# Kernel tuning notes

Hardware: AMD Instinct MI355X
Metric: run time of the kernel (lower is better)

The kernel has to match this reference:

```python
import jax, jax.numpy as jnp
import numpy as np

N = 100000      # nodes
E = 1600000     # edges
D = 64          # embedding_dim
NB = 5000       # boundary nodes
BLOCK = (8, 8, 8)
NBLK = BLOCK[0] * BLOCK[1] * BLOCK[2]  # 512 supernodes


def _segment_softmax(logits, seg, num):
    # jraph.segment_softmax: stable per-segment softmax
    m = jax.ops.segment_max(logits, seg, num_segments=num)
    e = jnp.exp(logits - m[seg])
    s = jax.ops.segment_sum(e, seg, num_segments=num)
    return e / s[seg]


def _gat(x, s, r, W, A, num):
    h = x @ W                       # [n, D]
    hs, hr = h[s], h[r]             # [E, D] gathers
    score = jax.nn.leaky_relu(jnp.concatenate([hs, hr], axis=-1) @ A)  # [E, 1]
    coeff = _segment_softmax(score, r, num)
    return jax.ops.segment_sum(hs * coeff, r, num_segments=num)        # [num, D]


def _graphnorm(x, gamma, beta, eps=1e-5):
    mean = jnp.mean(x, axis=0, keepdims=True)
    var = jnp.var(x, axis=0, keepdims=True)
    return gamma * (x - mean) / jnp.sqrt(var + eps) + beta


def setup_inputs() -> dict:
    key = jax.random.key(0)
    ks = jax.random.split(key, 16)

    def lecun(k, shape):
        return jax.random.normal(k, shape, jnp.float32) / jnp.sqrt(shape[0])

    return {
        "nodes": jax.random.normal(ks[0], (N, 7), jnp.float32),
        "senders": jax.random.randint(ks[1], (E,), 0, N, jnp.int32),
        "receivers": jax.random.randint(ks[2], (E,), 0, N, jnp.int32),
        "boundary_nodes": jax.random.randint(ks[3], (NB,), 0, N, jnp.int32),
        "disp_mean": jnp.zeros((3,), jnp.float32),
        "disp_std": jnp.ones((3,), jnp.float32),
        "embed_W": lecun(ks[4], (7, D)),
        "embed_b": jnp.zeros((D,), jnp.float32),
        "W1": lecun(ks[5], (D, D)),
        "A1": lecun(ks[6], (2 * D, 1)),
        "gamma1": jnp.ones((D,), jnp.float32),
        "beta1": jnp.zeros((D,), jnp.float32),
        "W2": lecun(ks[7], (D, D)),
        "A2": lecun(ks[8], (2 * D, 1)),
        "gamma2": jnp.ones((D,), jnp.float32),
        "beta2": jnp.zeros((D,), jnp.float32),
        "W3": lecun(ks[9], (D, D)),
        "A3": lecun(ks[10], (2 * D, 1)),
        "dec_W": lecun(ks[11], (D, 1)),
        "dec_b": jnp.zeros((1,), jnp.float32),
    }


def reference(nodes, senders, receivers, boundary_nodes, disp_mean, disp_std,
              embed_W, embed_b, W1, A1, gamma1, beta1, W2, A2, gamma2, beta2,
              W3, A3, dec_W, dec_b):
    coords = nodes[:, 0:3]
    # --- embedder: normalize boundary displacements, linear embed ---
    pos, disp, flag = nodes[:, 0:3], nodes[:, 3:6], nodes[:, 6:]
    b_disp = (disp[boundary_nodes] - disp_mean) / disp_std
    disp_n = disp.at[boundary_nodes].set(b_disp)
    x = jnp.concatenate([pos, disp_n, flag], axis=1) @ embed_W + embed_b  # [N, D]
    # --- GAT 1 + GraphNorm + silu + residual ---
    res1 = x
    x = _gat(x, senders, receivers, W1, A1, N)
    x = _graphnorm(x, gamma1, beta1)
    x = jax.nn.silu(x) + res1
    # --- BlockCoursening pooling ---
    dims = jnp.array(BLOCK)
    mn = jnp.min(coords, axis=0)
    mx = jnp.max(coords, axis=0)
    cell = (mx - mn) / dims
    gi = jnp.clip(jnp.floor((coords - mn) / cell).astype(jnp.int32), 0, dims - 1)
    bid = gi[:, 0] * (BLOCK[1] * BLOCK[2]) + gi[:, 1] * BLOCK[2] + gi[:, 2]  # [N]
    cnodes = jax.ops.segment_sum(x, bid, num_segments=NBLK)
    sizes = jax.ops.segment_sum(jnp.ones((N, 1), jnp.float32), bid, num_segments=NBLK)
    cnodes = cnodes / jnp.sqrt(sizes + 1e-10)
    bs, br = bid[senders], bid[receivers]
    # sorted-key dedup edge-weight mask (computed in source; unused by downstream GAT)
    keys = bs * NBLK + br
    idx = jnp.arange(E)
    sk, perm = jax.lax.sort_key_val(keys, idx)
    prev = jnp.concatenate([jnp.array([-1], sk.dtype), sk[:-1]])
    uniq = jnp.zeros((E,), bool).at[perm].set(sk != prev)
    edge_w = (uniq & (bs != br)).astype(jnp.float32)[:, None]  # noqa: F841 (dead in source too)
    # --- GAT 2 on coarsened graph + GraphNorm + silu + residual ---
    x2 = cnodes
    res2 = x2
    x2 = _gat(x2, bs, br, W2, A2, NBLK)
    x2 = _graphnorm(x2, gamma2, beta2)
    x2 = jax.nn.silu(x2) + res2
    # --- GAT 3 + residual ---
    res3 = x2
    x2 = _gat(x2, bs, br, W3, A3, NBLK)
    x2 = x2 + res3
    # --- decoder: sum-pool all nodes (single graph) -> linear -> scalar ---
    agg = jnp.sum(x2, axis=0, keepdims=True)  # segment_sum with one segment
    e = (agg @ dec_W + dec_b).squeeze()
    return e
```

## Files before the change

kernel.cpp:

```cpp
#include <hip/hip_runtime.h>
#include <hip/hip_bf16.h>

#define NN 100000
#define NE 1600000
#define NBN 5000
#define NCOARSE 512
#define NSB 391
#define NREP 8
#define NREP2 32

__device__ __forceinline__ unsigned f2ord(float f) {
    unsigned u = __float_as_uint(f);
    return (u & 0x80000000u) ? ~u : (u | 0x80000000u);
}
__device__ __forceinline__ float ord2f(unsigned u) {
    u = (u & 0x80000000u) ? (u & 0x7FFFFFFFu) : ~u;
    return __uint_as_float(u);
}
__device__ __forceinline__ float lrelu(float x) { return x > 0.f ? x : 0.01f * x; }

__global__ __launch_bounds__(256) void k_scatter(const int* __restrict__ bn, unsigned char* __restrict__ isb) {
    int i = blockIdx.x * 256 + threadIdx.x;
    if (i < NBN) isb[bn[i]] = 1;
}

__global__ __launch_bounds__(256) void k_embed(const float* __restrict__ nodes, const unsigned char* __restrict__ isb,
                                               const float* __restrict__ dmean, const float* __restrict__ dstd,
                                               const float* __restrict__ eW, const float* __restrict__ eb,
                                               float* __restrict__ x) {
    __shared__ float sW[448];
    __shared__ float sb[64];
    __shared__ float sm[3], sd[3];
    int t = threadIdx.x;
    for (int i = t; i < 448; i += 256) sW[i] = eW[i];
    if (t < 64) sb[t] = eb[t];
    if (t < 3) { sm[t] = dmean[t]; sd[t] = dstd[t]; }
    __syncthreads();
    int lane = t & 63, wv = t >> 6;
    int w = blockIdx.x * 4 + wv, nw = gridDim.x * 4;
    for (int n = w; n < NN; n += nw) {
        float row[7];
#pragma unroll
        for (int k = 0; k < 7; k++) row[k] = nodes[n * 7 + k];
        if (isb[n]) {
#pragma unroll
            for (int k = 0; k < 3; k++) row[3 + k] = (row[3 + k] - sm[k]) / sd[k];
        }
        float acc = sb[lane];
#pragma unroll
        for (int k = 0; k < 7; k++) acc += row[k] * sW[k * 64 + lane];
        x[n * 64 + lane] = acc;
    }
}

__global__ __launch_bounds__(256) void k_minmax(const float* __restrict__ nodes, unsigned* __restrict__ mn_ord,
                                                unsigned* __restrict__ mx_ord) {
    int tid = blockIdx.x * 256 + threadIdx.x;
    int stride = gridDim.x * 256;
    float mn[3] = {INFINITY, INFINITY, INFINITY};
    float mx[3] = {-INFINITY, -INFINITY, -INFINITY};
    for (int n = tid; n < NN; n += stride) {
#pragma unroll
        for (int k = 0; k < 3; k++) {
            float c = nodes[n * 7 + k];
            mn[k] = fminf(mn[k], c);
            mx[k] = fmaxf(mx[k], c);
        }
    }
#pragma unroll
    for (int off = 32; off; off >>= 1) {
#pragma unroll
        for (int k = 0; k < 3; k++) {
            mn[k] = fminf(mn[k], __shfl_down(mn[k], off));
            mx[k] = fmaxf(mx[k], __shfl_down(mx[k], off));
        }
    }
    if ((threadIdx.x & 63) == 0) {
#pragma unroll
        for (int k = 0; k < 3; k++) {
            atomicMin(&mn_ord[k], f2ord(mn[k]));
            atomicMax(&mx_ord[k], f2ord(mx[k]));
        }
    }
}

__global__ __launch_bounds__(256) void k_bid(const float* __restrict__ nodes, const unsigned* __restrict__ mn_ord,
                                             const unsigned* __restrict__ mx_ord, int* __restrict__ bid) {
    int n = blockIdx.x * 256 + threadIdx.x;
    if (n >= NN) return;
    int g[3];
#pragma unroll
    for (int k = 0; k < 3; k++) {
        float mn = ord2f(mn_ord[k]), mx = ord2f(mx_ord[k]);
        float cell = (mx - mn) / 8.0f;
        int gi = (int)floorf((nodes[n * 7 + k] - mn) / cell);
        gi = gi < 0 ? 0 : (gi > 7 ? 7 : gi);
        g[k] = gi;
    }
    bid[n] = g[0] * 64 + g[1] * 8 + g[2];
}

__global__ __launch_bounds__(256) void k_mm(const float* __restrict__ x, const float* __restrict__ W,
                                            const float* __restrict__ A, float* __restrict__ h,
                                            float* __restrict__ as_, float* __restrict__ ar_, int nrow) {
    __shared__ float sW[4096];
    __shared__ float sA[128];
    int t = threadIdx.x;
    for (int i = t; i < 4096; i += 256) sW[i] = W[i];
    if (t < 128) sA[t] = A[t];
    __syncthreads();
    int lane = t & 63, wv = t >> 6;
    int w = blockIdx.x * 4 + wv, nw = gridDim.x * 4;
    for (int n = w; n < nrow; n += nw) {
        const float* xr = x + (size_t)n * 64;
        float acc = 0.f;
#pragma unroll
        for (int k = 0; k < 64; k++) acc += xr[k] * sW[k * 64 + lane];
        h[(size_t)n * 64 + lane] = acc;
        float va = acc * sA[lane], vr = acc * sA[64 + lane];
#pragma unroll
        for (int off = 32; off; off >>= 1) {
            va += __shfl_down(va, off);
            vr += __shfl_down(vr, off);
        }
        if (lane == 0) { as_[n] = va; ar_[n] = vr; }
    }
}

__global__ __launch_bounds__(256) void k_deg(const int* __restrict__ re, unsigned* __restrict__ deg) {
    int e = blockIdx.x * 256 + threadIdx.x;
    if (e < NE) atomicAdd(&deg[re[e]], 1u);
}

__global__ __launch_bounds__(256) void k_scan1(const unsigned* __restrict__ deg, unsigned* __restrict__ rowptr,
                                               unsigned* __restrict__ partial) {
    __shared__ unsigned s[256];
    int t = threadIdx.x, i = blockIdx.x * 256 + t;
    unsigned v = (i < NN) ? deg[i] : 0u;
    s[t] = v;
    __syncthreads();
    for (int off = 1; off < 256; off <<= 1) {
        unsigned u = (t >= off) ? s[t - off] : 0u;
        __syncthreads();
        s[t] += u;
        __syncthreads();
    }
    if (i < NN) rowptr[i] = s[t] - v;
    if (t == 255) partial[blockIdx.x] = s[255];
}

__global__ __launch_bounds__(512) void k_scan2(unsigned* __restrict__ partial) {
    __shared__ unsigned s[512];
    int t = threadIdx.x;
    unsigned v = (t < NSB) ? partial[t] : 0u;
    s[t] = v;
    __syncthreads();
    for (int off = 1; off < 512; off <<= 1) {
        unsigned u = (t >= off) ? s[t - off] : 0u;
        __syncthreads();
        s[t] += u;
        __syncthreads();
    }
    if (t < NSB) partial[t] = s[t] - v;
}

__global__ __launch_bounds__(256) void k_scan3(unsigned* __restrict__ rowptr, const unsigned* __restrict__ partial,
                                               unsigned* __restrict__ cursor) {
    int t = threadIdx.x, i = blockIdx.x * 256 + t;
    if (i < NN) {
        unsigned r = rowptr[i] + partial[blockIdx.x];
        rowptr[i] = r;
        cursor[i] = r;
    }
    if (i == 0) rowptr[NN] = NE;
}

__global__ __launch_bounds__(256) void k_fill(const int* __restrict__ se, const int* __restrict__ re,
                                              unsigned* __restrict__ cursor, int* __restrict__ csr_s) {
    int e = blockIdx.x * 256 + threadIdx.x;
    if (e >= NE) return;
    unsigned pos = atomicAdd(&cursor[re[e]], 1u);
    atomicExch(&csr_s[pos], se[e]);
}

__global__ __launch_bounds__(256) void k_gat1(const unsigned* __restrict__ rowptr, const int* __restrict__ csr_s,
                                              const float* __restrict__ as_, const float* __restrict__ ar_,
                                              const float* __restrict__ h, float* __restrict__ o_raw) {
    int t = threadIdx.x, lane = t & 63, wv = t >> 6;
    int r = blockIdx.x * 4 + wv;
    int g = lane >> 4, fl = lane & 15;
    int p0 = rowptr[r], p1 = rowptr[r + 1];
    float arj = ar_[r];
    float m = -INFINITY, ss = 0.f;
    float a0 = 0.f, a1 = 0.f, a2 = 0.f, a3 = 0.f;
    int p = p0 + g;
    int s = (p < p1) ? csr_s[p] : 0;
    while (p < p1) {
        int pn = p + 4;
        int sn = (pn < p1) ? csr_s[pn] : 0;
        float sc = lrelu(as_[s] + arj);
        const float4 hv = *(const float4*)(h + (size_t)s * 64 + fl * 4);
        float newm = fmaxf(m, sc);
        float scale = __expf(m - newm);
        float w = __expf(sc - newm);
        ss = ss * scale + w;
        a0 = a0 * scale + w * hv.x;
        a1 = a1 * scale + w * hv.y;
        a2 = a2 * scale + w * hv.z;
        a3 = a3 * scale + w * hv.w;
        m = newm;
        p = pn;
        s = sn;
    }
#pragma unroll
    for (int off = 16; off < 64; off <<= 1) {
        float m2 = __shfl_xor(m, off);
        float ss2 = __shfl_xor(ss, off);
        float b0 = __shfl_xor(a0, off), b1 = __shfl_xor(a1, off);
        float b2 = __shfl_xor(a2, off), b3 = __shfl_xor(a3, off);
        float M = fmaxf(m, m2);
        float e1 = (M == -INFINITY) ? 0.f : __expf(m - M);
        float e2 = (M == -INFINITY) ? 0.f : __expf(m2 - M);
        ss = ss * e1 + ss2 * e2;
        a0 = a0 * e1 + b0 * e2;
        a1 = a1 * e1 + b1 * e2;
        a2 = a2 * e1 + b2 * e2;
        a3 = a3 * e1 + b3 * e2;
        m = M;
    }
    if (g == 0) {
        float inv = ss > 0.f ? 1.f / ss : 0.f;
        float4 v = make_float4(a0 * inv, a1 * inv, a2 * inv, a3 * inv);
        *(float4*)(o_raw + (size_t)r * 64 + fl * 4) = v;
    }
}

__global__ __launch_bounds__(256) void k_stats2(const float* __restrict__ o_raw,
                                                float* __restrict__ colsum, float* __restrict__ colsq) {
    __shared__ float l1[4][64], l2[4][64];
    int t = threadIdx.x, lane = t & 63, wv = t >> 6;
    int w = blockIdx.x * 4 + wv, nw = gridDim.x * 4;
    float cs = 0.f, cq = 0.f;
    for (int n = w; n < NN; n += nw) {
        float v = o_raw[(size_t)n * 64 + lane];
        cs += v;
        cq += v * v;
    }
    l1[wv][lane] = cs;
    l2[wv][lane] = cq;
    __syncthreads();
    if (wv == 0) {
        float a = l1[0][lane] + l1[1][lane] + l1[2][lane] + l1[3][lane];
        float b = l2[0][lane] + l2[1][lane] + l2[2][lane] + l2[3][lane];
        unsafeAtomicAdd(&colsum[lane], a);
        unsafeAtomicAdd(&colsq[lane], b);
    }
}

__global__ void k_meanvar(const float* __restrict__ colsum, const float* __restrict__ colsq, float* __restrict__ mr) {
    int t = threadIdx.x;
    if (t < 64) {
        float mean = colsum[t] / (float)NN;
        float var = colsq[t] / (float)NN - mean * mean;
        mr[t] = mean;
        mr[64 + t] = rsqrtf(var + 1e-5f);
    }
}

__global__ __launch_bounds__(256) void k_apply(const float* __restrict__ o_raw, const float* __restrict__ res1,
                                               const float* __restrict__ gamma, const float* __restrict__ beta,
                                               const float* __restrict__ mr, float* __restrict__ x1) {
    int t = threadIdx.x, lane = t & 63;
    int n = blockIdx.x * 4 + (t >> 6);
    if (n >= NN) return;
    float v = o_raw[(size_t)n * 64 + lane];
    float y = gamma[lane] * (v - mr[lane]) * mr[64 + lane] + beta[lane];
    float s = y / (1.f + __expf(-y));
    x1[(size_t)n * 64 + lane] = s + res1[(size_t)n * 64 + lane];
}

__global__ __launch_bounds__(256) void k_deg2(const int* __restrict__ bid, unsigned* __restrict__ deg2r) {
    int n = blockIdx.x * 256 + threadIdx.x;
    if (n < NN) atomicAdd(&deg2r[(n & (NREP2 - 1)) * NCOARSE + bid[n]], 1u);
}

__global__ __launch_bounds__(512) void k_scanb(const unsigned* __restrict__ deg2r, unsigned* __restrict__ rowptr2,
                                               unsigned* __restrict__ cursor2r, unsigned* __restrict__ deg2) {
    __shared__ unsigned s[512];
    int b = threadIdx.x;
    unsigned tot = 0;
    for (int r = 0; r < NREP2; r++) tot += deg2r[r * NCOARSE + b];
    deg2[b] = tot;
    s[b] = tot;
    __syncthreads();
    for (int off = 1; off < 512; off <<= 1) {
        unsigned u = (b >= off) ? s[b - off] : 0u;
        __syncthreads();
        s[b] += u;
        __syncthreads();
    }
    unsigned base = s[b] - tot;
    rowptr2[b] = base;
    if (b == 0) rowptr2[NCOARSE] = NN;
    unsigned run = base;
    for (int r = 0; r < NREP2; r++) {
        cursor2r[r * NCOARSE + b] = run;
        run += deg2r[r * NCOARSE + b];
    }
}

__global__ __launch_bounds__(256) void k_fill2(const int* __restrict__ bid, unsigned* __restrict__ cursor2r,
                                               int* __restrict__ csr_n) {
    int n = blockIdx.x * 256 + threadIdx.x;
    if (n >= NN) return;
    unsigned pos = atomicAdd(&cursor2r[(n & (NREP2 - 1)) * NCOARSE + bid[n]], 1u);
    atomicExch(&csr_n[pos], n);
}

__global__ __launch_bounds__(256) void k_cnacc(const int* __restrict__ csr_n, const int* __restrict__ bid,
                                               const float* __restrict__ x1, float* __restrict__ cnacc) {
    int t = threadIdx.x, lane = t & 63, wv = t >> 6;
    int q0 = (blockIdx.x * 4 + wv) * 64;
    if (q0 >= NN) return;
    int q1 = q0 + 64 < NN ? q0 + 64 : NN;
    int n = csr_n[q0];
    int cur = bid[n];
    float acc = 0.f;
    for (int q = q0; q < q1; q++) {
        int n2 = (q + 1 < q1) ? csr_n[q + 1] : 0;
        int b2 = (q + 1 < q1) ? bid[n2] : -1;
        acc += x1[(size_t)n * 64 + lane];
        if (b2 != cur) {
            unsafeAtomicAdd(&cnacc[cur * 64 + lane], acc);
            acc = 0.f;
            cur = b2;
        }
        n = n2;
    }
}

__global__ __launch_bounds__(256) void k_cnscale(const float* __restrict__ cnacc, const unsigned* __restrict__ deg2,
                                                 float* __restrict__ x2) {
    int t = threadIdx.x, lane = t & 63;
    int b = blockIdx.x * 4 + (t >> 6);
    if (b >= NCOARSE) return;
    x2[b * 64 + lane] = cnacc[b * 64 + lane] / sqrtf((float)deg2[b] + 1e-10f);
}

__global__ __launch_bounds__(256) void k_cnt(const int* __restrict__ se, const int* __restrict__ re,
                                             const int* __restrict__ bid, unsigned* __restrict__ cntr) {
    int e = blockIdx.x * 256 + threadIdx.x;
    if (e >= NE) return;
    int rep = e & (NREP - 1);
    atomicAdd(&cntr[(size_t)rep * NCOARSE * NCOARSE + bid[re[e]] * NCOARSE + bid[se[e]]], 1u);
}

__global__ __launch_bounds__(256) void k_cntmerge(const unsigned* __restrict__ cntr, unsigned* __restrict__ cnt) {
    int i = blockIdx.x * 256 + threadIdx.x;
    unsigned s = 0;
#pragma unroll
    for (int r = 0; r < NREP; r++) s += cntr[(size_t)r * NCOARSE * NCOARSE + i];
    cnt[i] = s;
}

__global__ __launch_bounds__(256) void k_cgat(const float* __restrict__ h, const float* __restrict__ as_,
                                              const float* __restrict__ ar_, const unsigned* __restrict__ cnt,
                                              float* __restrict__ g) {
    __shared__ float red[256];
    __shared__ float sw[NCOARSE];
    __shared__ float acc_s[4][64];
    int t = threadIdx.x, lane = t & 63, wv = t >> 6;
    int j = blockIdx.x;
    float arj = ar_[j];
    unsigned c0 = cnt[j * NCOARSE + t], c1 = cnt[j * NCOARSE + t + 256];
    float s0 = lrelu(as_[t] + arj), s1 = lrelu(as_[t + 256] + arj);
    float v0 = c0 ? s0 : -INFINITY, v1 = c1 ? s1 : -INFINITY;
    red[t] = fmaxf(v0, v1);
    __syncthreads();
    for (int off = 128; off; off >>= 1) {
        if (t < off) red[t] = fmaxf(red[t], red[t + off]);
        __syncthreads();
    }
    float m = red[0];
    __syncthreads();
    float w0 = c0 ? (float)c0 * __expf(s0 - m) : 0.f;
    float w1 = c1 ? (float)c1 * __expf(s1 - m) : 0.f;
    sw[t] = w0;
    sw[t + 256] = w1;
    red[t] = w0 + w1;
    __syncthreads();
    for (int off = 128; off; off >>= 1) {
        if (t < off) red[t] += red[t + off];
        __syncthreads();
    }
    float ss = red[0];
    float acc = 0.f;
    int i0 = wv * 128;
#pragma unroll 4
    for (int i = i0; i < i0 + 128; i++) acc += sw[i] * h[i * 64 + lane];
    acc_s[wv][lane] = acc;
    __syncthreads();
    if (wv == 0) {
        float tot = acc_s[0][lane] + acc_s[1][lane] + acc_s[2][lane] + acc_s[3][lane];
        g[j * 64 + lane] = ss > 0.f ? tot / ss : 0.f;
    }
}

__global__ __launch_bounds__(64) void k_cnorm(const float* __restrict__ gin, const float* __restrict__ gamma,
                                              const float* __restrict__ beta, const float* __restrict__ res,
                                              float* __restrict__ xout) {
    int f = blockIdx.x, lane = threadIdx.x;
    float v[8];
    float s = 0.f, q = 0.f;
#pragma unroll
    for (int k = 0; k < 8; k++) {
        v[k] = gin[(lane + 64 * k) * 64 + f];
        s += v[k];
        q += v[k] * v[k];
    }
#pragma unroll
    for (int off = 32; off; off >>= 1) {
        s += __shfl_down(s, off);
        q += __shfl_down(q, off);
    }
    s = __shfl(s, 0);
    q = __shfl(q, 0);
    float mean = s / 512.f, var = q / 512.f - mean * mean, rstd = rsqrtf(var + 1e-5f);
    float gf = gamma[f], bf = beta[f];
#pragma unroll
    for (int k = 0; k < 8; k++) {
        float y = gf * (v[k] - mean) * rstd + bf;
        float si = y / (1.f + __expf(-y));
        int idx = (lane + 64 * k) * 64 + f;
        xout[idx] = si + res[idx];
    }
}

__global__ __launch_bounds__(256) void k_final(const float* __restrict__ g3, const float* __restrict__ x3,
                                               const float* __restrict__ dW, const float* __restrict__ db,
                                               float* __restrict__ out) {
    __shared__ float l[4];
    int t = threadIdx.x;
    float p = 0.f;
    for (int idx = t; idx < NCOARSE * 64; idx += 256) p += (g3[idx] + x3[idx]) * dW[idx & 63];
#pragma unroll
    for (int off = 32; off; off >>= 1) p += __shfl_down(p, off);
    if ((t & 63) == 0) l[t >> 6] = p;
    __syncthreads();
    if (t == 0) out[0] = l[0] + l[1] + l[2] + l[3] + db[0];
}

extern "C" void kernel_launch(void* const* d_in, const int* in_sizes, int n_in,
                              void* d_out, int out_size, void* d_ws, size_t ws_size,
                              hipStream_t stream) {
    const float* nodes = (const float*)d_in[0];
    const int* senders = (const int*)d_in[1];
    const int* receivers = (const int*)d_in[2];
    const int* bnodes = (const int*)d_in[3];
    const float* dmean = (const float*)d_in[4];
    const float* dstd = (const float*)d_in[5];
    const float* eW = (const float*)d_in[6];
    const float* eb = (const float*)d_in[7];
    const float* W1 = (const float*)d_in[8];
    const float* A1 = (const float*)d_in[9];
    const float* gamma1 = (const float*)d_in[10];
    const float* beta1 = (const float*)d_in[11];
    const float* W2 = (const float*)d_in[12];
    const float* A2 = (const float*)d_in[13];
    const float* gamma2 = (const float*)d_in[14];
    const float* beta2 = (const float*)d_in[15];
    const float* W3 = (const float*)d_in[16];
    const float* A3 = (const float*)d_in[17];
    const float* dW = (const float*)d_in[18];
    const float* db = (const float*)d_in[19];
    float* out = (float*)d_out;

    char* p = (char*)d_ws;
    auto alloc = [&](size_t b) { char* r = p; p += (b + 255) & ~(size_t)255; return r; };
    float* x_emb = (float*)alloc((size_t)NN * 64 * 4);
    float* h1 = (float*)alloc((size_t)NN * 64 * 4);
    float* o_raw = (float*)alloc((size_t)NN * 64 * 4);
    float* as1 = (float*)alloc(NN * 4);
    float* ar1 = (float*)alloc(NN * 4);
    int* bid = (int*)alloc(NN * 4);
    unsigned char* isb = (unsigned char*)alloc(NN);
    float* colsum = (float*)alloc(64 * 4);
    float* colsq = (float*)alloc(64 * 4);
    float* mr = (float*)alloc(128 * 4);
    unsigned* mn_ord = (unsigned*)alloc(3 * 4);
    unsigned* mx_ord = (unsigned*)alloc(3 * 4);
    unsigned* cnt = (unsigned*)alloc((size_t)NCOARSE * NCOARSE * 4);
    unsigned* cntr = (unsigned*)alloc((size_t)NREP * NCOARSE * NCOARSE * 4);
    float* cnacc = (float*)alloc(NCOARSE * 64 * 4);
    float* x2 = (float*)alloc(NCOARSE * 64 * 4);
    float* h2 = (float*)alloc(NCOARSE * 64 * 4);
    float* as2 = (float*)alloc(NCOARSE * 4);
    float* ar2 = (float*)alloc(NCOARSE * 4);
    float* gat2 = (float*)alloc(NCOARSE * 64 * 4);
    float* x3 = (float*)alloc(NCOARSE * 64 * 4);
    float* h3 = (float*)alloc(NCOARSE * 64 * 4);
    float* as3 = (float*)alloc(NCOARSE * 4);
    float* ar3 = (float*)alloc(NCOARSE * 4);
    float* gat3 = (float*)alloc(NCOARSE * 64 * 4);
    unsigned* deg = (unsigned*)alloc(NN * 4);
    unsigned* rowptr = (unsigned*)alloc((NN + 1) * 4);
    unsigned* cursor = (unsigned*)alloc(NN * 4);
    unsigned* partial = (unsigned*)alloc(512 * 4);
    int* csr_s = (int*)alloc((size_t)NE * 4);
    unsigned* deg2r = (unsigned*)alloc((size_t)NREP2 * NCOARSE * 4);
    unsigned* deg2 = (unsigned*)alloc(NCOARSE * 4);
    unsigned* rowptr2 = (unsigned*)alloc((NCOARSE + 1) * 4);
    unsigned* cursor2r = (unsigned*)alloc((size_t)NREP2 * NCOARSE * 4);
    int* csr_n = (int*)alloc(NN * 4);

    hipMemsetAsync(isb, 0, NN, stream);
    hipMemsetAsync(colsum, 0, 64 * 4, stream);
    hipMemsetAsync(colsq, 0, 64 * 4, stream);
    hipMemsetAsync(mn_ord, 0xFF, 12, stream);
    hipMemsetAsync(mx_ord, 0, 12, stream);
    hipMemsetAsync(cntr, 0, (size_t)NREP * NCOARSE * NCOARSE * 4, stream);
    hipMemsetAsync(cnacc, 0, NCOARSE * 64 * 4, stream);
    hipMemsetAsync(deg, 0, NN * 4, stream);
    hipMemsetAsync(deg2r, 0, (size_t)NREP2 * NCOARSE * 4, stream);

    k_scatter<<<(NBN + 255) / 256, 256, 0, stream>>>(bnodes, isb);
    k_embed<<<2048, 256, 0, stream>>>(nodes, isb, dmean, dstd, eW, eb, x_emb);
    k_minmax<<<512, 256, 0, stream>>>(nodes, mn_ord, mx_ord);
    k_bid<<<(NN + 255) / 256, 256, 0, stream>>>(nodes, mn_ord, mx_ord, bid);
    k_deg<<<(NE + 255) / 256, 256, 0, stream>>>(receivers, deg);
    k_scan1<<<NSB, 256, 0, stream>>>(deg, rowptr, partial);
    k_scan2<<<1, 512, 0, stream>>>(partial);
    k_scan3<<<NSB, 256, 0, stream>>>(rowptr, partial, cursor);
    k_fill<<<(NE + 255) / 256, 256, 0, stream>>>(senders, receivers, cursor, csr_s);
    k_deg2<<<(NN + 255) / 256, 256, 0, stream>>>(bid, deg2r);
    k_scanb<<<1, 512, 0, stream>>>(deg2r, rowptr2, cursor2r, deg2);
    k_fill2<<<(NN + 255) / 256, 256, 0, stream>>>(bid, cursor2r, csr_n);
    k_cnt<<<(NE + 255) / 256, 256, 0, stream>>>(senders, receivers, bid, cntr);
    k_cntmerge<<<NCOARSE * NCOARSE / 256, 256, 0, stream>>>(cntr, cnt);
    k_mm<<<2048, 256, 0, stream>>>(x_emb, W1, A1, h1, as1, ar1, NN);
    k_gat1<<<NN / 4, 256, 0, stream>>>(rowptr, csr_s, as1, ar1, h1, o_raw);
    k_stats2<<<512, 256, 0, stream>>>(o_raw, colsum, colsq);
    k_meanvar<<<1, 64, 0, stream>>>(colsum, colsq, mr);
    k_apply<<<NN / 4, 256, 0, stream>>>(o_raw, x_emb, gamma1, beta1, mr, h1);
    k_cnacc<<<NSB, 256, 0, stream>>>(csr_n, bid, h1, cnacc);
    k_cnscale<<<NCOARSE / 4, 256, 0, stream>>>(cnacc, deg2, x2);
    k_mm<<<NCOARSE / 4, 256, 0, stream>>>(x2, W2, A2, h2, as2, ar2, NCOARSE);
    k_cgat<<<NCOARSE, 256, 0, stream>>>(h2, as2, ar2, cnt, gat2);
    k_cnorm<<<64, 64, 0, stream>>>(gat2, gamma2, beta2, x2, x3);
    k_mm<<<NCOARSE / 4, 256, 0, stream>>>(x3, W3, A3, h3, as3, ar3, NCOARSE);
    k_cgat<<<NCOARSE, 256, 0, stream>>>(h3, as3, ar3, cnt, gat3);
    k_final<<<1, 256, 0, stream>>>(gat3, x3, dW, db, out);
}
```

Measured before the change: 806.4 us.

## Replace atomic CSR fill with two-pass bucketed counting sort by receiver

The old CSR build did one global atomicAdd per edge on a per-node cursor and scattered sender ids to random positions. The new version first partitions edges into buckets of 512 receivers, using shared-memory histograms and one global atomic per bucket per tile. It then sorts within each bucket using shared-memory cursors, so global writes stay within a local region. It also swaps atomicExch for plain stores in fill2. The cost is two extra 6.4 MB intermediate arrays and an extra pass over the edges, and pass2 runs with only 196 blocks.

```diff
diff --git a/kernel.cpp b/kernel.cpp
--- a/kernel.cpp
+++ b/kernel.cpp
@@ -8,6 +8,8 @@
 #define NSB 391
 #define NREP 8
 #define NREP2 32
+#define NBUCK 196
+#define P1TILE 8192
 
 __device__ __forceinline__ unsigned f2ord(float f) {
     unsigned u = __float_as_uint(f);
@@ -164,23 +166,63 @@
     if (t < NSB) partial[t] = s[t] - v;
 }
 
-__global__ __launch_bounds__(256) void k_scan3(unsigned* __restrict__ rowptr, const unsigned* __restrict__ partial,
-                                               unsigned* __restrict__ cursor) {
+__global__ __launch_bounds__(256) void k_scan3(unsigned* __restrict__ rowptr, const unsigned* __restrict__ partial) {
     int t = threadIdx.x, i = blockIdx.x * 256 + t;
-    if (i < NN) {
-        unsigned r = rowptr[i] + partial[blockIdx.x];
-        rowptr[i] = r;
-        cursor[i] = r;
-    }
+    if (i < NN) rowptr[i] += partial[blockIdx.x];
     if (i == 0) rowptr[NN] = NE;
 }
 
-__global__ __launch_bounds__(256) void k_fill(const int* __restrict__ se, const int* __restrict__ re,
-                                              unsigned* __restrict__ cursor, int* __restrict__ csr_s) {
-    int e = blockIdx.x * 256 + threadIdx.x;
-    if (e >= NE) return;
-    unsigned pos = atomicAdd(&cursor[re[e]], 1u);
-    atomicExch(&csr_s[pos], se[e]);
+__global__ void k_gcinit(const unsigned* __restrict__ rowptr, unsigned* __restrict__ gcur) {
+    int b = threadIdx.x;
+    if (b < NBUCK) gcur[b] = rowptr[b << 9];
+}
+
+__global__ __launch_bounds__(256) void k_pass1(const int* __restrict__ se, const int* __restrict__ re,
+                                               unsigned* __restrict__ gcur, int* __restrict__ pairSe,
+                                               int* __restrict__ pairRe) {
+    __shared__ unsigned hist[NBUCK], cur[NBUCK], gbase[NBUCK];
+    int t = threadIdx.x;
+    int e0 = blockIdx.x * P1TILE;
+    for (int i = t; i < NBUCK; i += 256) { hist[i] = 0; cur[i] = 0; }
+    __syncthreads();
+    for (int i = t; i < P1TILE; i += 256) {
+        int e = e0 + i;
+        if (e < NE) atomicAdd(&hist[re[e] >> 9], 1u);
+    }
+    __syncthreads();
+    for (int i = t; i < NBUCK; i += 256) gbase[i] = atomicAdd(&gcur[i], hist[i]);
+    __syncthreads();
+    for (int i = t; i < P1TILE; i += 256) {
+        int e = e0 + i;
+        if (e < NE) {
+            int r = re[e];
+            int b = r >> 9;
+            unsigned j = atomicAdd(&cur[b], 1u);
+            unsigned pos = gbase[b] + j;
+            pairSe[pos] = se[e];
+            pairRe[pos] = r;
+        }
+    }
+}
+
+__global__ __launch_bounds__(256) void k_pass2(const unsigned* __restrict__ rowptr, const int* __restrict__ pairSe,
+                                               const int* __restrict__ pairRe, int* __restrict__ csr_s) {
+    __shared__ unsigned cur[512];
+    int t = threadIdx.x;
+    int r0 = blockIdx.x << 9;
+    for (int i = t; i < 512; i += 256) {
+        int r = r0 + i;
+        cur[i] = (r < NN) ? rowptr[r] : 0u;
+    }
+    __syncthreads();
+    unsigned p0 = rowptr[r0];
+    int rend = r0 + 512 < NN ? r0 + 512 : NN;
+    unsigned p1 = rowptr[rend];
+    for (unsigned p = p0 + t; p < p1; p += 256) {
+        int r = pairRe[p];
+        unsigned pos = atomicAdd(&cur[r - r0], 1u);
+        csr_s[pos] = pairSe[p];
+    }
 }
 
 __global__ __launch_bounds__(256) void k_gat1(const unsigned* __restrict__ rowptr, const int* __restrict__ csr_s,
@@ -314,7 +356,7 @@
     int n = blockIdx.x * 256 + threadIdx.x;
     if (n >= NN) return;
     unsigned pos = atomicAdd(&cursor2r[(n & (NREP2 - 1)) * NCOARSE + bid[n]], 1u);
-    atomicExch(&csr_n[pos], n);
+    csr_n[pos] = n;
 }
 
 __global__ __launch_bounds__(256) void k_cnacc(const int* __restrict__ csr_n, const int* __restrict__ bid,
@@ -504,9 +546,11 @@
     float* gat3 = (float*)alloc(NCOARSE * 64 * 4);
     unsigned* deg = (unsigned*)alloc(NN * 4);
     unsigned* rowptr = (unsigned*)alloc((NN + 1) * 4);
-    unsigned* cursor = (unsigned*)alloc(NN * 4);
     unsigned* partial = (unsigned*)alloc(512 * 4);
     int* csr_s = (int*)alloc((size_t)NE * 4);
+    int* pairSe = (int*)alloc((size_t)NE * 4);
+    int* pairRe = (int*)alloc((size_t)NE * 4);
+    unsigned* gcur = (unsigned*)alloc(NBUCK * 4);
     unsigned* deg2r = (unsigned*)alloc((size_t)NREP2 * NCOARSE * 4);
     unsigned* deg2 = (unsigned*)alloc(NCOARSE * 4);
     unsigned* rowptr2 = (unsigned*)alloc((NCOARSE + 1) * 4);
@@ -530,8 +574,10 @@
     k_deg<<<(NE + 255) / 256, 256, 0, stream>>>(receivers, deg);
     k_scan1<<<NSB, 256, 0, stream>>>(deg, rowptr, partial);
     k_scan2<<<1, 512, 0, stream>>>(partial);
-    k_scan3<<<NSB, 256, 0, stream>>>(rowptr, partial, cursor);
-    k_fill<<<(NE + 255) / 256, 256, 0, stream>>>(senders, receivers, cursor, csr_s);
+    k_scan3<<<NSB, 256, 0, stream>>>(rowptr, partial);
+    k_gcinit<<<1, 256, 0, stream>>>(rowptr, gcur);
+    k_pass1<<<(NE + P1TILE - 1) / P1TILE, 256, 0, stream>>>(senders, receivers, gcur, pairSe, pairRe);
+    k_pass2<<<NBUCK, 256, 0, stream>>>(rowptr, pairSe, pairRe, csr_s);
     k_deg2<<<(NN + 255) / 256, 256, 0, stream>>>(bid, deg2r);
     k_scanb<<<1, 512, 0, stream>>>(deg2r, rowptr2, cursor2r, deg2);
     k_fill2<<<(NN + 255) / 256, 256, 0, stream>>>(bid, cursor2r, csr_n);
```

Result: faster. 740.2 us (-8.2%).
